# Kernel optimization log

Measured on AMD Instinct MI355X. Metric: run time of the kernel, lower is better.

The kernel has to match this reference:

```python
import jax, jax.numpy as jnp
import numpy as np
import math

EPS = 1e-06
H = 16


def favorplus_features(x, proj, eps=EPS):
    # x: [B,h,T,dk], proj: [h,m,dk] -> [B,h,T,m]
    xw = jnp.einsum('bhtd,hmd->bhtm', x, proj)
    xw = xw - jnp.max(xw, axis=-1, keepdims=True)
    exp_part = jnp.exp(xw)
    x_norm_sq = jnp.sum(x * x, axis=-1, keepdims=True)
    base = jnp.exp(-0.5 * x_norm_sq)
    return exp_part * base + eps


def setup_inputs() -> dict:
    key = jax.random.key(0)
    ks = jax.random.split(key, 7)
    B, T, d = 4, 4096, 1024
    h, m = H, 256
    dk = d // h
    s = 1.0 / math.sqrt(d)  # keep activations O(1) so exp(-0.5||q||^2) is meaningful
    return {
        'x': jax.random.normal(ks[0], (B, T, d), jnp.float32),
        'Wq': jax.random.normal(ks[1], (d, d), jnp.float32) * s,
        'Wk': jax.random.normal(ks[2], (d, d), jnp.float32) * s,
        'Wv': jax.random.normal(ks[3], (d, d), jnp.float32) * s,
        'Wo': jax.random.normal(ks[4], (d, d), jnp.float32) * s,
        'bo': jnp.zeros((d,), jnp.float32),
        'proj': jax.random.normal(ks[5], (h, m, dk), jnp.float32),
    }


def reference(x, Wq, Wk, Wv, Wo, bo, proj):
    B, T, d = x.shape
    h = H
    dk = d // h
    m = proj.shape[1]

    def heads(W):
        # torch Linear: x @ W.T ; split heads -> [B,h,T,dk]
        return (x @ W.T).reshape(B, T, h, dk).transpose(0, 2, 1, 3)

    Q, K, V = heads(Wq), heads(Wk), heads(Wv)
    scale = 1.0 / math.sqrt(dk)
    phiQ = favorplus_features(Q * scale, proj) / math.sqrt(m)  # [B,h,T,m]
    phiK = favorplus_features(K * scale, proj) / math.sqrt(m)

    KV = jnp.einsum('bhtm,bhtd->bhmd', phiK, V)          # [B,h,m,dk]
    Ksum = jnp.sum(phiK, axis=2)                          # [B,h,m]
    num = jnp.einsum('bhtm,bhmd->bhtd', phiQ, KV)         # [B,h,T,dk]
    den = jnp.einsum('bhtm,bhm->bht', phiQ, Ksum)[..., None] + EPS
    out_heads = num / den                                  # [B,h,T,dk]
    merged = out_heads.transpose(0, 2, 1, 3).reshape(B, T, h * dk)
    return merged @ Wo.T + bo
```

## Files before the change

### kernel.cpp

```cpp
#include <hip/hip_runtime.h>

typedef unsigned short u16;
typedef __attribute__((ext_vector_type(8))) short s8v;
typedef __attribute__((ext_vector_type(4))) float f4v;
typedef __attribute__((ext_vector_type(8))) unsigned short u16x8;
typedef __attribute__((ext_vector_type(4))) unsigned short u16x4;

__device__ __forceinline__ float b2f(u16 u) {
  unsigned int v = ((unsigned int)u) << 16;
  float f;
  __builtin_memcpy(&f, &v, 4);
  return f;
}
__device__ __forceinline__ u16 f2b(float f) {
  unsigned int v;
  __builtin_memcpy(&v, &f, 4);
  v = v + 0x7fffu + ((v >> 16) & 1u);
  return (u16)(v >> 16);
}
__device__ __forceinline__ void gl_lds16(const void* g, void* l) {
  __builtin_amdgcn_global_load_lds((__attribute__((address_space(1))) void*)g,
                                   (__attribute__((address_space(3))) void*)l,
                                   16, 0, 0);
}
__device__ __forceinline__ f4v mfma16(s8v a, s8v b, f4v c) {
  return __builtin_amdgcn_mfma_f32_16x16x32_bf16(a, b, c, 0, 0, 0);
}

__global__ __launch_bounds__(256) void k_convert(
    const float* __restrict__ x, const float* __restrict__ wq,
    const float* __restrict__ wk, const float* __restrict__ wv,
    const float* __restrict__ wo, const float* __restrict__ proj,
    u16* __restrict__ xb, u16* __restrict__ wqb, u16* __restrict__ wkb,
    u16* __restrict__ wvb, u16* __restrict__ wob, u16* __restrict__ projb) {
  const int NX = 4194304, NW = 262144, NP = 65536;
  const int total = NX + 4 * NW + NP;
  for (int i = blockIdx.x * 256 + threadIdx.x; i < total; i += gridDim.x * 256) {
    const float* src;
    u16* dst;
    int off;
    float scale = 1.0f;
    if (i < NX) { src = x; dst = xb; off = i; }
    else if (i < NX + NW) { src = wq; dst = wqb; off = i - NX; }
    else if (i < NX + 2 * NW) { src = wk; dst = wkb; off = i - NX - NW; }
    else if (i < NX + 3 * NW) { src = wv; dst = wvb; off = i - NX - 2 * NW; }
    else if (i < NX + 4 * NW) { src = wo; dst = wob; off = i - NX - 3 * NW; }
    else { src = proj; dst = projb; off = i - NX - 4 * NW; scale = 0.125f; }
    const float4 v = reinterpret_cast<const float4*>(src)[off];
    u16x4 o;
    o[0] = f2b(v.x * scale); o[1] = f2b(v.y * scale);
    o[2] = f2b(v.z * scale); o[3] = f2b(v.w * scale);
    reinterpret_cast<u16x4*>(dst)[off] = o;
  }
}

template <int COUTF32, int NCB>
__global__ __launch_bounds__(256) void k_gemm_swz(
    const u16* __restrict__ A, const u16* __restrict__ W,
    void* __restrict__ Cq, void* __restrict__ Ck, void* __restrict__ Cv,
    const float* __restrict__ bias) {
  const int bid = blockIdx.x;
  const int xcd = bid & 7, slot = bid >> 3;
  const int yg = slot / NCB, cb = slot - yg * NCB;
  const long row0 = (long)(yg * 8 + xcd) * 128;
  const int wrow0 = cb * 128;
  void* C = (cb < 8) ? Cq : (cb < 16) ? Ck : Cv;
  const int col0 = (cb & 7) * 128;
  __shared__ u16 As[128 * 64];
  __shared__ u16 Bs[128 * 64];
  const int tid = threadIdx.x, w = tid >> 6, l = tid & 63;
  const int wr = w >> 1, wc = w & 1, fr = l & 15, fq = l >> 4;
  f4v acc[4][4];
#pragma unroll
  for (int i = 0; i < 4; ++i)
#pragma unroll
    for (int j = 0; j < 4; ++j) acc[i][j] = 0.f;
  const int lr = l >> 3, lc = l & 7;
  for (int kt = 0; kt < 16; ++kt) {
    const int k0 = kt << 6;
    __syncthreads();
#pragma unroll
    for (int q = 0; q < 4; ++q) {
      const int r = q * 32 + w * 8 + lr;
      const int sc = (lc ^ (r & 7)) << 3;
      gl_lds16(A + (row0 + r) * 1024L + k0 + sc, (char*)As + q * 4096 + w * 1024);
      gl_lds16(W + (wrow0 + r) * 1024L + k0 + sc, (char*)Bs + q * 4096 + w * 1024);
    }
    __syncthreads();
#pragma unroll
    for (int ks = 0; ks < 2; ++ks) {
      s8v af[4], bf[4];
#pragma unroll
      for (int i = 0; i < 4; ++i) {
        const int R = wr * 64 + i * 16 + fr;
        af[i] = *(const s8v*)&As[R * 64 + (((ks * 4 + fq) ^ (R & 7)) << 3)];
      }
#pragma unroll
      for (int j = 0; j < 4; ++j) {
        const int R = wc * 64 + j * 16 + fr;
        bf[j] = *(const s8v*)&Bs[R * 64 + (((ks * 4 + fq) ^ (R & 7)) << 3)];
      }
#pragma unroll
      for (int i = 0; i < 4; ++i)
#pragma unroll
        for (int j = 0; j < 4; ++j) acc[i][j] = mfma16(af[i], bf[j], acc[i][j]);
    }
  }
  if (COUTF32) {
#pragma unroll
    for (int j = 0; j < 4; ++j) {
      const int col = col0 + wc * 64 + j * 16 + fr;
      const float bv = bias ? bias[col] : 0.f;
#pragma unroll
      for (int i = 0; i < 4; ++i) {
        const long row = row0 + wr * 64 + i * 16 + fq * 4;
#pragma unroll
        for (int r = 0; r < 4; ++r)
          ((float*)C)[(row + r) * 1024L + col] = acc[i][j][r] + bv;
      }
    }
  } else {
    __syncthreads();
    u16* myl = As + w * 1024;
    const int rr2 = l >> 2, c2 = (l & 3) * 16;
#pragma unroll
    for (int i = 0; i < 4; ++i) {
#pragma unroll
      for (int j = 0; j < 4; ++j)
#pragma unroll
        for (int r = 0; r < 4; ++r)
          myl[(fq * 4 + r) * 64 + j * 16 + fr] = f2b(acc[i][j][r]);
      const u16x8 o0 = *(const u16x8*)&myl[rr2 * 64 + c2];
      const u16x8 o1 = *(const u16x8*)&myl[rr2 * 64 + c2 + 8];
      u16* dst = (u16*)C + (row0 + wr * 64 + i * 16 + rr2) * 1024L + col0 + wc * 64 + c2;
      *(u16x8*)dst = o0;
      *(u16x8*)(dst + 8) = o1;
    }
  }
}

__global__ __launch_bounds__(512) void k_kvfused(
    const u16* __restrict__ Kb, const u16* __restrict__ Vb,
    const u16* __restrict__ projb, float* __restrict__ kvp,
    float* __restrict__ ksp) {
  __shared__ u16 Ps[256 * 72];
  __shared__ u16 PhiT[256 * 136];
  __shared__ u16 Ks[128 * 72];
  __shared__ u16 VT[64 * 136];
  __shared__ float norms[128];
  const int tid = threadIdx.x, w = tid >> 6, l = tid & 63;
  const int fr = l & 15, fq = l >> 4;
  const int c = blockIdx.x, bh = blockIdx.y, b = bh >> 4, h = bh & 15;
#pragma unroll
  for (int q = 0; q < 4; ++q) {
    const int flat = q * 4096 + tid * 8;
    const int m = flat >> 6, cc = flat & 63;
    *(u16x8*)&Ps[m * 72 + cc] = *(const u16x8*)&projb[h * 16384 + flat];
  }
  f4v kacc[2][4];
  float ksum = 0.f;
#pragma unroll
  for (int i = 0; i < 2; ++i)
#pragma unroll
    for (int j = 0; j < 4; ++j) kacc[i][j] = 0.f;
  const int kr = tid >> 3, kc = (tid & 7) * 8;
  const int vt = tid >> 2, ve0 = (tid & 3) * 16;
  const long kbase = (long)b * 4096 + (long)c * 1024;
  u16x8 ck0 = *(const u16x8*)&Kb[(kbase + kr) * 1024 + h * 64 + kc];
  u16x8 ck1 = *(const u16x8*)&Kb[(kbase + 64 + kr) * 1024 + h * 64 + kc];
  u16x8 cv0 = *(const u16x8*)&Vb[(kbase + vt) * 1024 + h * 64 + ve0];
  u16x8 cv1 = *(const u16x8*)&Vb[(kbase + vt) * 1024 + h * 64 + ve0 + 8];
  for (int it = 0; it < 8; ++it) {
    __syncthreads();
    *(u16x8*)&Ks[kr * 72 + kc] = ck0;
    *(u16x8*)&Ks[(64 + kr) * 72 + kc] = ck1;
#pragma unroll
    for (int jj = 0; jj < 8; ++jj) VT[(ve0 + jj) * 136 + vt] = cv0[jj];
#pragma unroll
    for (int jj = 0; jj < 8; ++jj) VT[(ve0 + 8 + jj) * 136 + vt] = cv1[jj];
    __syncthreads();
    if (it < 7) {
      const long t0n = kbase + (it + 1) * 128;
      ck0 = *(const u16x8*)&Kb[(t0n + kr) * 1024 + h * 64 + kc];
      ck1 = *(const u16x8*)&Kb[(t0n + 64 + kr) * 1024 + h * 64 + kc];
      cv0 = *(const u16x8*)&Vb[(t0n + vt) * 1024 + h * 64 + ve0];
      cv1 = *(const u16x8*)&Vb[(t0n + vt) * 1024 + h * 64 + ve0 + 8];
    }
    {
      const int row = tid >> 2, part = tid & 3;
      const u16x8 a0 = *(const u16x8*)&Ks[row * 72 + part * 16];
      const u16x8 a1 = *(const u16x8*)&Ks[row * 72 + part * 16 + 8];
      float s = 0.f;
#pragma unroll
      for (int jj = 0; jj < 8; ++jj) { const float v = b2f(a0[jj]); s += v * v; }
#pragma unroll
      for (int jj = 0; jj < 8; ++jj) { const float v = b2f(a1[jj]); s += v * v; }
      s += __shfl_xor(s, 1);
      s += __shfl_xor(s, 2);
      if (part == 0) norms[row] = s * 0.015625f;
    }
    f4v pacc[16];
#pragma unroll
    for (int f = 0; f < 16; ++f) pacc[f] = 0.f;
#pragma unroll
    for (int ks = 0; ks < 2; ++ks) {
      const s8v a = *(const s8v*)&Ks[(w * 16 + fr) * 72 + ks * 32 + fq * 8];
#pragma unroll
      for (int f = 0; f < 16; ++f) {
        const s8v bb = *(const s8v*)&Ps[(f * 16 + fr) * 72 + ks * 32 + fq * 8];
        pacc[f] = mfma16(a, bb, pacc[f]);
      }
    }
    __syncthreads();
    float mx[4] = {-3.4e38f, -3.4e38f, -3.4e38f, -3.4e38f};
#pragma unroll
    for (int f = 0; f < 16; ++f)
#pragma unroll
      for (int r = 0; r < 4; ++r) mx[r] = fmaxf(mx[r], pacc[f][r]);
#pragma unroll
    for (int sft = 1; sft < 16; sft <<= 1)
#pragma unroll
      for (int r = 0; r < 4; ++r) mx[r] = fmaxf(mx[r], __shfl_xor(mx[r], sft));
    float nsq[4];
#pragma unroll
    for (int r = 0; r < 4; ++r) nsq[r] = norms[w * 16 + fq * 4 + r];
#pragma unroll
    for (int f = 0; f < 16; ++f) {
      u16x4 o;
#pragma unroll
      for (int r = 0; r < 4; ++r)
        o[r] = f2b((__expf(pacc[f][r] - mx[r] - 0.5f * nsq[r]) + 1e-6f) * 0.0625f);
      *(u16x4*)&PhiT[(f * 16 + fr) * 136 + w * 16 + fq * 4] = o;
    }
    __syncthreads();
#pragma unroll
    for (int ks = 0; ks < 4; ++ks) {
      s8v af[2], bf[4];
#pragma unroll
      for (int i = 0; i < 2; ++i)
        af[i] = *(const s8v*)&PhiT[(w * 32 + i * 16 + fr) * 136 + ks * 32 + fq * 8];
#pragma unroll
      for (int j = 0; j < 4; ++j)
        bf[j] = *(const s8v*)&VT[(j * 16 + fr) * 136 + ks * 32 + fq * 8];
#pragma unroll
      for (int i = 0; i < 2; ++i)
#pragma unroll
        for (int j = 0; j < 4; ++j) kacc[i][j] = mfma16(af[i], bf[j], kacc[i][j]);
    }
    if (tid < 256) {
#pragma unroll
      for (int t8 = 0; t8 < 16; ++t8) {
        const u16x8 p = *(const u16x8*)&PhiT[tid * 136 + t8 * 8];
#pragma unroll
        for (int jj = 0; jj < 8; ++jj) ksum += b2f(p[jj]);
      }
    }
  }
  const long obase = (long)(c * 64 + bh) * 16384;
#pragma unroll
  for (int i = 0; i < 2; ++i) {
    const int m = w * 32 + i * 16 + fq * 4;
#pragma unroll
    for (int j = 0; j < 4; ++j)
#pragma unroll
      for (int r = 0; r < 4; ++r)
        kvp[obase + (long)(m + r) * 64 + j * 16 + fr] = kacc[i][j][r];
  }
  if (tid < 256) ksp[(long)(c * 64 + bh) * 256 + tid] = ksum;
}

__global__ __launch_bounds__(256) void k_red(
    const float* __restrict__ kvp, const float* __restrict__ ksp,
    u16* __restrict__ KVT, float* __restrict__ ksumf) {
  const int bh = blockIdx.x, qq = blockIdx.y, tid = threadIdx.x;
  for (int it = 0; it < 16; ++it) {
    const int idx = (qq * 16 + it) * 256 + tid;
    const int m = idx >> 6, e = idx & 63;
    float s = 0.f;
#pragma unroll
    for (int cc = 0; cc < 4; ++cc)
      s += kvp[(long)(cc * 64 + bh) * 16384 + (long)m * 64 + e];
    KVT[(long)bh * 16384 + (long)e * 256 + m] = f2b(s);
  }
  if (qq == 0) {
    float s = 0.f;
#pragma unroll
    for (int cc = 0; cc < 4; ++cc) s += ksp[(long)(cc * 64 + bh) * 256 + tid];
    ksumf[bh * 256 + tid] = s;
  }
}

__global__ __launch_bounds__(512) void k_numfused(
    const u16* __restrict__ Qb, const u16* __restrict__ projb,
    const u16* __restrict__ KVT, const float* __restrict__ ksumf,
    u16* __restrict__ merged) {
  __shared__ u16 Ps[256 * 72];
  __shared__ u16 Qs[128 * 72];
  __shared__ u16 Phi[128 * 264];
  __shared__ u16 Bs[64 * 264];
  __shared__ float ksl[256];
  __shared__ float denA[128];
  __shared__ float norms[128];
  const int tid = threadIdx.x, w = tid >> 6, l = tid & 63;
  const int fr = l & 15, fq = l >> 4;
  const int tt = blockIdx.x, bh = blockIdx.y, b = bh >> 4, h = bh & 15;
#pragma unroll
  for (int q = 0; q < 4; ++q) {
    const int flat = q * 4096 + tid * 8;
    const int m = flat >> 6, cc = flat & 63;
    *(u16x8*)&Ps[m * 72 + cc] = *(const u16x8*)&projb[h * 16384 + flat];
  }
#pragma unroll
  for (int q = 0; q < 2; ++q) {
    const int flat = q * 4096 + tid * 8;
    const int r = flat >> 6, cc = flat & 63;
    *(u16x8*)&Qs[r * 72 + cc] =
        *(const u16x8*)&Qb[((long)b * 4096 + tt * 128 + r) * 1024 + h * 64 + cc];
  }
  {
    const int e = tid >> 3, seg = (tid & 7) * 32;
#pragma unroll
    for (int k = 0; k < 4; ++k) {
      const u16x8 vv = *(const u16x8*)&KVT[(long)bh * 16384 + e * 256 + seg + k * 8];
      *(u16x8*)&Bs[e * 264 + seg + k * 8] = vv;
    }
  }
  if (tid < 256) ksl[tid] = ksumf[bh * 256 + tid];
  __syncthreads();
  {
    const int row = tid >> 2, part = tid & 3;
    const u16x8 a0 = *(const u16x8*)&Qs[row * 72 + part * 16];
    const u16x8 a1 = *(const u16x8*)&Qs[row * 72 + part * 16 + 8];
    float s = 0.f;
#pragma unroll
    for (int jj = 0; jj < 8; ++jj) { const float v = b2f(a0[jj]); s += v * v; }
#pragma unroll
    for (int jj = 0; jj < 8; ++jj) { const float v = b2f(a1[jj]); s += v * v; }
    s += __shfl_xor(s, 1);
    s += __shfl_xor(s, 2);
    if (part == 0) norms[row] = s * 0.015625f;
  }
  f4v pacc[16];
#pragma unroll
  for (int f = 0; f < 16; ++f) pacc[f] = 0.f;
#pragma unroll
  for (int ks = 0; ks < 2; ++ks) {
    const s8v a = *(const s8v*)&Qs[(w * 16 + fr) * 72 + ks * 32 + fq * 8];
#pragma unroll
    for (int f = 0; f < 16; ++f) {
      const s8v bb = *(const s8v*)&Ps[(f * 16 + fr) * 72 + ks * 32 + fq * 8];
      pacc[f] = mfma16(a, bb, pacc[f]);
    }
  }
  __syncthreads();
  float mx[4] = {-3.4e38f, -3.4e38f, -3.4e38f, -3.4e38f};
#pragma unroll
  for (int f = 0; f < 16; ++f)
#pragma unroll
    for (int r = 0; r < 4; ++r) mx[r] = fmaxf(mx[r], pacc[f][r]);
#pragma unroll
  for (int sft = 1; sft < 16; sft <<= 1)
#pragma unroll
    for (int r = 0; r < 4; ++r) mx[r] = fmaxf(mx[r], __shfl_xor(mx[r], sft));
  float nsq[4];
#pragma unroll
  for (int r = 0; r < 4; ++r) nsq[r] = norms[w * 16 + fq * 4 + r];
#pragma unroll
  for (int f = 0; f < 16; ++f)
#pragma unroll
    for (int r = 0; r < 4; ++r)
      Phi[(w * 16 + fq * 4 + r) * 264 + f * 16 + fr] =
          f2b((__expf(pacc[f][r] - mx[r] - 0.5f * nsq[r]) + 1e-6f) * 0.0625f);
  __syncthreads();
  {
    const int row = tid >> 2, part = tid & 3;
    float d = 0.f;
#pragma unroll
    for (int j8 = 0; j8 < 8; ++j8) {
      const u16x8 p = *(const u16x8*)&Phi[row * 264 + part * 64 + j8 * 8];
      const float4 k0 = *(const float4*)&ksl[part * 64 + j8 * 8];
      const float4 k1 = *(const float4*)&ksl[part * 64 + j8 * 8 + 4];
      d += b2f(p[0]) * k0.x; d += b2f(p[1]) * k0.y;
      d += b2f(p[2]) * k0.z; d += b2f(p[3]) * k0.w;
      d += b2f(p[4]) * k1.x; d += b2f(p[5]) * k1.y;
      d += b2f(p[6]) * k1.z; d += b2f(p[7]) * k1.w;
    }
    d += __shfl_xor(d, 1);
    d += __shfl_xor(d, 2);
    if (part == 0) denA[row] = d;
  }
  f4v acc[4];
#pragma unroll
  for (int j = 0; j < 4; ++j) acc[j] = 0.f;
#pragma unroll
  for (int kt = 0; kt < 8; ++kt) {
    const s8v af = *(const s8v*)&Phi[(w * 16 + fr) * 264 + kt * 32 + fq * 8];
#pragma unroll
    for (int j = 0; j < 4; ++j) {
      const s8v bb = *(const s8v*)&Bs[(j * 16 + fr) * 264 + kt * 32 + fq * 8];
      acc[j] = mfma16(af, bb, acc[j]);
    }
  }
  __syncthreads();
#pragma unroll
  for (int r = 0; r < 4; ++r) {
    const float rd = 1.0f / (denA[w * 16 + fq * 4 + r] + 1e-6f);
    const long t = (long)tt * 128 + w * 16 + fq * 4 + r;
    const long gb = ((long)b * 4096 + t) * 1024 + h * 64;
#pragma unroll
    for (int j = 0; j < 4; ++j)
      merged[gb + j * 16 + fr] = f2b(acc[j][r] * rd);
  }
}

extern "C" void kernel_launch(void* const* d_in, const int* in_sizes, int n_in,
                              void* d_out, int out_size, void* d_ws, size_t ws_size,
                              hipStream_t stream) {
  const float* x = (const float*)d_in[0];
  const float* Wq = (const float*)d_in[1];
  const float* Wk = (const float*)d_in[2];
  const float* Wv = (const float*)d_in[3];
  const float* Wo = (const float*)d_in[4];
  const float* bo = (const float*)d_in[5];
  const float* proj = (const float*)d_in[6];
  char* ws = (char*)d_ws;
  u16* Vout = (u16*)d_out;
  u16* xb = (u16*)(ws + 0L);
  u16* wqb = (u16*)(ws + 33554432L);
  u16* wkb = (u16*)(ws + 35651584L);
  u16* wvb = (u16*)(ws + 37748736L);
  u16* wob = (u16*)(ws + 39845888L);
  u16* projb = (u16*)(ws + 41943040L);
  u16* Qb = (u16*)(ws + 42467328L);
  u16* Kb = (u16*)(ws + 76021760L);
  u16* KVT = (u16*)(ws + 109576192L);
  float* ksumf = (float*)(ws + 111673344L);
  float* kvp = (float*)xb;
  float* ksp = (float*)(ws + 16777216L);
  u16* merged = Kb;
  (void)in_sizes; (void)n_in; (void)out_size; (void)ws_size;

  k_convert<<<dim3(2048), dim3(256), 0, stream>>>(x, Wq, Wk, Wv, Wo, proj,
                                                  xb, wqb, wkb, wvb, wob, projb);
  k_gemm_swz<0, 24><<<dim3(3072), dim3(256), 0, stream>>>(
      xb, wqb, Qb, Kb, Vout, nullptr);
  k_kvfused<<<dim3(4, 64), dim3(512), 0, stream>>>(Kb, Vout, projb, kvp, ksp);
  k_red<<<dim3(64, 4), dim3(256), 0, stream>>>(kvp, ksp, KVT, ksumf);
  k_numfused<<<dim3(32, 64), dim3(512), 0, stream>>>(Qb, projb, KVT, ksumf, merged);
  k_gemm_swz<1, 8><<<dim3(1024), dim3(256), 0, stream>>>(
      merged, wob, d_out, d_out, d_out, bo);
}
```

Before: 332.8 us.

## Make numerator kernel wave-independent with per-wave tiles and persistent looping

The numerator kernel is restructured so each wave loads its own Q rows straight from global memory into MFMA registers, computes the features, the denominator (folded into the feature write) and the numerator product in a per-wave LDS tile. This removes the block-wide barriers. Each block now loops over 8 tiles of 16 rows per wave with register prefetch of the next Q tile, and the grid shrinks from 2048 to 256 blocks. Output goes out through LDS as vectorized stores. In the KV kernel, row norms now come from lane shuffles instead of shared memory plus a barrier. The smaller grid means less parallelism to hide latency, and each block reloads the projection and KV less often.

```diff
diff --git a/kernel.cpp b/kernel.cpp
--- a/kernel.cpp
+++ b/kernel.cpp
@@ -147,7 +147,6 @@
   __shared__ u16 PhiT[256 * 136];
   __shared__ u16 Ks[128 * 72];
   __shared__ u16 VT[64 * 136];
-  __shared__ float norms[128];
   const int tid = threadIdx.x, w = tid >> 6, l = tid & 63;
   const int fr = l & 15, fq = l >> 4;
   const int c = blockIdx.x, bh = blockIdx.y, b = bh >> 4, h = bh & 15;
@@ -186,8 +185,9 @@
       cv0 = *(const u16x8*)&Vb[(t0n + vt) * 1024 + h * 64 + ve0];
       cv1 = *(const u16x8*)&Vb[(t0n + vt) * 1024 + h * 64 + ve0 + 8];
     }
+    float nrm;
     {
-      const int row = tid >> 2, part = tid & 3;
+      const int row = w * 16 + (l >> 2), part = l & 3;
       const u16x8 a0 = *(const u16x8*)&Ks[row * 72 + part * 16];
       const u16x8 a1 = *(const u16x8*)&Ks[row * 72 + part * 16 + 8];
       float s = 0.f;
@@ -197,7 +197,7 @@
       for (int jj = 0; jj < 8; ++jj) { const float v = b2f(a1[jj]); s += v * v; }
       s += __shfl_xor(s, 1);
       s += __shfl_xor(s, 2);
-      if (part == 0) norms[row] = s * 0.015625f;
+      nrm = s * 0.015625f;
     }
     f4v pacc[16];
 #pragma unroll
@@ -211,7 +211,6 @@
         pacc[f] = mfma16(a, bb, pacc[f]);
       }
     }
-    __syncthreads();
     float mx[4] = {-3.4e38f, -3.4e38f, -3.4e38f, -3.4e38f};
 #pragma unroll
     for (int f = 0; f < 16; ++f)
@@ -223,7 +222,7 @@
       for (int r = 0; r < 4; ++r) mx[r] = fmaxf(mx[r], __shfl_xor(mx[r], sft));
     float nsq[4];
 #pragma unroll
-    for (int r = 0; r < 4; ++r) nsq[r] = norms[w * 16 + fq * 4 + r];
+    for (int r = 0; r < 4; ++r) nsq[r] = __shfl(nrm, (fq * 4 + r) * 4);
 #pragma unroll
     for (int f = 0; f < 16; ++f) {
       u16x4 o;
@@ -295,121 +294,109 @@
     const u16* __restrict__ KVT, const float* __restrict__ ksumf,
     u16* __restrict__ merged) {
   __shared__ u16 Ps[256 * 72];
-  __shared__ u16 Qs[128 * 72];
-  __shared__ u16 Phi[128 * 264];
   __shared__ u16 Bs[64 * 264];
+  __shared__ u16 PhiW[8][16 * 264];
   __shared__ float ksl[256];
-  __shared__ float denA[128];
-  __shared__ float norms[128];
   const int tid = threadIdx.x, w = tid >> 6, l = tid & 63;
   const int fr = l & 15, fq = l >> 4;
-  const int tt = blockIdx.x, bh = blockIdx.y, b = bh >> 4, h = bh & 15;
+  const int tq = blockIdx.x, bh = blockIdx.y, b = bh >> 4, h = bh & 15;
 #pragma unroll
   for (int q = 0; q < 4; ++q) {
     const int flat = q * 4096 + tid * 8;
-    const int m = flat >> 6, cc = flat & 63;
-    *(u16x8*)&Ps[m * 72 + cc] = *(const u16x8*)&projb[h * 16384 + flat];
-  }
-#pragma unroll
-  for (int q = 0; q < 2; ++q) {
-    const int flat = q * 4096 + tid * 8;
-    const int r = flat >> 6, cc = flat & 63;
-    *(u16x8*)&Qs[r * 72 + cc] =
-        *(const u16x8*)&Qb[((long)b * 4096 + tt * 128 + r) * 1024 + h * 64 + cc];
+    *(u16x8*)&Ps[(flat >> 6) * 72 + (flat & 63)] =
+        *(const u16x8*)&projb[h * 16384 + flat];
   }
   {
     const int e = tid >> 3, seg = (tid & 7) * 32;
 #pragma unroll
-    for (int k = 0; k < 4; ++k) {
-      const u16x8 vv = *(const u16x8*)&KVT[(long)bh * 16384 + e * 256 + seg + k * 8];
-      *(u16x8*)&Bs[e * 264 + seg + k * 8] = vv;
-    }
+    for (int k = 0; k < 4; ++k)
+      *(u16x8*)&Bs[e * 264 + seg + k * 8] =
+          *(const u16x8*)&KVT[(long)bh * 16384 + e * 256 + seg + k * 8];
   }
   if (tid < 256) ksl[tid] = ksumf[bh * 256 + tid];
+  u16* Pw = &PhiW[w][0];
+  const long tbase = (long)b * 4096 + tq * 1024 + w * 128;
+  const u16* qrow = Qb + (tbase + fr) * 1024 + h * 64 + fq * 8;
+  s8v a0 = *(const s8v*)&qrow[0];
+  s8v a1 = *(const s8v*)&qrow[32];
   __syncthreads();
-  {
-    const int row = tid >> 2, part = tid & 3;
-    const u16x8 a0 = *(const u16x8*)&Qs[row * 72 + part * 16];
-    const u16x8 a1 = *(const u16x8*)&Qs[row * 72 + part * 16 + 8];
+  for (int n = 0; n < 8; ++n) {
+    s8v n0, n1;
+    if (n < 7) {
+      n0 = *(const s8v*)&qrow[(long)(n + 1) * 16 * 1024];
+      n1 = *(const s8v*)&qrow[(long)(n + 1) * 16 * 1024 + 32];
+    }
     float s = 0.f;
 #pragma unroll
-    for (int jj = 0; jj < 8; ++jj) { const float v = b2f(a0[jj]); s += v * v; }
-#pragma unroll
-    for (int jj = 0; jj < 8; ++jj) { const float v = b2f(a1[jj]); s += v * v; }
-    s += __shfl_xor(s, 1);
-    s += __shfl_xor(s, 2);
-    if (part == 0) norms[row] = s * 0.015625f;
-  }
-  f4v pacc[16];
-#pragma unroll
-  for (int f = 0; f < 16; ++f) pacc[f] = 0.f;
-#pragma unroll
-  for (int ks = 0; ks < 2; ++ks) {
-    const s8v a = *(const s8v*)&Qs[(w * 16 + fr) * 72 + ks * 32 + fq * 8];
+    for (int jj = 0; jj < 8; ++jj) { const float v = b2f((u16)a0[jj]); s += v * v; }
+#pragma unroll
+    for (int jj = 0; jj < 8; ++jj) { const float v = b2f((u16)a1[jj]); s += v * v; }
+    s += __shfl_xor(s, 16);
+    s += __shfl_xor(s, 32);
+    s *= 0.015625f;
+    f4v pacc[16];
+#pragma unroll
+    for (int f = 0; f < 16; ++f) pacc[f] = 0.f;
+#pragma unroll
+    for (int f = 0; f < 16; ++f)
+      pacc[f] = mfma16(a0, *(const s8v*)&Ps[(f * 16 + fr) * 72 + fq * 8], pacc[f]);
+#pragma unroll
+    for (int f = 0; f < 16; ++f)
+      pacc[f] = mfma16(a1, *(const s8v*)&Ps[(f * 16 + fr) * 72 + 32 + fq * 8], pacc[f]);
+    float mx[4] = {-3.4e38f, -3.4e38f, -3.4e38f, -3.4e38f};
+#pragma unroll
+    for (int f = 0; f < 16; ++f)
+#pragma unroll
+      for (int r = 0; r < 4; ++r) mx[r] = fmaxf(mx[r], pacc[f][r]);
+#pragma unroll
+    for (int sft = 1; sft < 16; sft <<= 1)
+#pragma unroll
+      for (int r = 0; r < 4; ++r) mx[r] = fmaxf(mx[r], __shfl_xor(mx[r], sft));
+    float nsq[4];
+#pragma unroll
+    for (int r = 0; r < 4; ++r) nsq[r] = __shfl(s, fq * 4 + r);
+    float dp[4] = {0.f, 0.f, 0.f, 0.f};
 #pragma unroll
     for (int f = 0; f < 16; ++f) {
-      const s8v bb = *(const s8v*)&Ps[(f * 16 + fr) * 72 + ks * 32 + fq * 8];
-      pacc[f] = mfma16(a, bb, pacc[f]);
-    }
-  }
-  __syncthreads();
-  float mx[4] = {-3.4e38f, -3.4e38f, -3.4e38f, -3.4e38f};
-#pragma unroll
-  for (int f = 0; f < 16; ++f)
-#pragma unroll
-    for (int r = 0; r < 4; ++r) mx[r] = fmaxf(mx[r], pacc[f][r]);
-#pragma unroll
-  for (int sft = 1; sft < 16; sft <<= 1)
-#pragma unroll
-    for (int r = 0; r < 4; ++r) mx[r] = fmaxf(mx[r], __shfl_xor(mx[r], sft));
-  float nsq[4];
-#pragma unroll
-  for (int r = 0; r < 4; ++r) nsq[r] = norms[w * 16 + fq * 4 + r];
-#pragma unroll
-  for (int f = 0; f < 16; ++f)
-#pragma unroll
-    for (int r = 0; r < 4; ++r)
-      Phi[(w * 16 + fq * 4 + r) * 264 + f * 16 + fr] =
-          f2b((__expf(pacc[f][r] - mx[r] - 0.5f * nsq[r]) + 1e-6f) * 0.0625f);
-  __syncthreads();
-  {
-    const int row = tid >> 2, part = tid & 3;
-    float d = 0.f;
-#pragma unroll
-    for (int j8 = 0; j8 < 8; ++j8) {
-      const u16x8 p = *(const u16x8*)&Phi[row * 264 + part * 64 + j8 * 8];
-      const float4 k0 = *(const float4*)&ksl[part * 64 + j8 * 8];
-      const float4 k1 = *(const float4*)&ksl[part * 64 + j8 * 8 + 4];
-      d += b2f(p[0]) * k0.x; d += b2f(p[1]) * k0.y;
-      d += b2f(p[2]) * k0.z; d += b2f(p[3]) * k0.w;
-      d += b2f(p[4]) * k1.x; d += b2f(p[5]) * k1.y;
-      d += b2f(p[6]) * k1.z; d += b2f(p[7]) * k1.w;
-    }
-    d += __shfl_xor(d, 1);
-    d += __shfl_xor(d, 2);
-    if (part == 0) denA[row] = d;
-  }
-  f4v acc[4];
-#pragma unroll
-  for (int j = 0; j < 4; ++j) acc[j] = 0.f;
-#pragma unroll
-  for (int kt = 0; kt < 8; ++kt) {
-    const s8v af = *(const s8v*)&Phi[(w * 16 + fr) * 264 + kt * 32 + fq * 8];
-#pragma unroll
-    for (int j = 0; j < 4; ++j) {
-      const s8v bb = *(const s8v*)&Bs[(j * 16 + fr) * 264 + kt * 32 + fq * 8];
-      acc[j] = mfma16(af, bb, acc[j]);
-    }
-  }
-  __syncthreads();
-#pragma unroll
-  for (int r = 0; r < 4; ++r) {
-    const float rd = 1.0f / (denA[w * 16 + fq * 4 + r] + 1e-6f);
-    const long t = (long)tt * 128 + w * 16 + fq * 4 + r;
-    const long gb = ((long)b * 4096 + t) * 1024 + h * 64;
+      const float kv = ksl[f * 16 + fr];
+#pragma unroll
+      for (int r = 0; r < 4; ++r) {
+        const u16 pb = f2b((__expf(pacc[f][r] - mx[r] - 0.5f * nsq[r]) + 1e-6f) * 0.0625f);
+        Pw[(fq * 4 + r) * 264 + f * 16 + fr] = pb;
+        dp[r] += b2f(pb) * kv;
+      }
+    }
+#pragma unroll
+    for (int sft = 1; sft < 16; sft <<= 1)
+#pragma unroll
+      for (int r = 0; r < 4; ++r) dp[r] += __shfl_xor(dp[r], sft);
+    float rd[4];
+#pragma unroll
+    for (int r = 0; r < 4; ++r) rd[r] = 1.0f / (dp[r] + 1e-6f);
+    f4v acc[4];
+#pragma unroll
+    for (int j = 0; j < 4; ++j) acc[j] = 0.f;
+#pragma unroll
+    for (int kt = 0; kt < 8; ++kt) {
+      const s8v af = *(const s8v*)&Pw[fr * 264 + kt * 32 + fq * 8];
+#pragma unroll
+      for (int j = 0; j < 4; ++j)
+        acc[j] = mfma16(af, *(const s8v*)&Bs[(j * 16 + fr) * 264 + kt * 32 + fq * 8], acc[j]);
+    }
 #pragma unroll
     for (int j = 0; j < 4; ++j)
-      merged[gb + j * 16 + fr] = f2b(acc[j][r] * rd);
+#pragma unroll
+      for (int r = 0; r < 4; ++r)
+        Pw[(fq * 4 + r) * 264 + j * 16 + fr] = f2b(acc[j][r] * rd[r]);
+    {
+      const u16x8 o0 = *(const u16x8*)&Pw[(l >> 2) * 264 + (l & 3) * 16];
+      const u16x8 o1 = *(const u16x8*)&Pw[(l >> 2) * 264 + (l & 3) * 16 + 8];
+      u16* dst = merged + (tbase + n * 16 + (l >> 2)) * 1024 + h * 64 + (l & 3) * 16;
+      *(u16x8*)dst = o0;
+      *(u16x8*)(dst + 8) = o1;
+    }
+    a0 = n0;
+    a1 = n1;
   }
 }
 
@@ -446,7 +433,7 @@
       xb, wqb, Qb, Kb, Vout, nullptr);
   k_kvfused<<<dim3(4, 64), dim3(512), 0, stream>>>(Kb, Vout, projb, kvp, ksp);
   k_red<<<dim3(64, 4), dim3(256), 0, stream>>>(kvp, ksp, KVT, ksumf);
-  k_numfused<<<dim3(32, 64), dim3(512), 0, stream>>>(Qb, projb, KVT, ksumf, merged);
+  k_numfused<<<dim3(4, 64), dim3(512), 0, stream>>>(Qb, projb, KVT, ksumf, merged);
   k_gemm_swz<1, 8><<<dim3(1024), dim3(256), 0, stream>>>(
       merged, wob, d_out, d_out, d_out, bo);
 }
```

Result: faster. 306.5 us, median of 2 (-7.9%).
